# Kernel tuning notes

Hardware: AMD Instinct MI355X
Metric: run time of the kernel (lower is better)

The kernel has to match this reference:

```python
import jax, jax.numpy as jnp
import numpy as np

D = 1024
H = 16
HD = D // H
SCALE = HD ** -0.5


def setup_inputs() -> dict:
    key = jax.random.key(0)
    ks = jax.random.split(key, 5)
    x = jax.random.normal(ks[0], (2, 2048, D), dtype=jnp.float32)
    s = 1.0 / np.sqrt(D)
    W_qkv = jax.random.uniform(ks[1], (D, 3 * D), jnp.float32, -s, s)
    b_qkv = jax.random.uniform(ks[2], (3 * D,), jnp.float32, -s, s)
    W_out = jax.random.uniform(ks[3], (D, D), jnp.float32, -s, s)
    b_out = jax.random.uniform(ks[4], (D,), jnp.float32, -s, s)
    return {"x": x, "W_qkv": W_qkv, "b_qkv": b_qkv, "W_out": W_out, "b_out": b_out}


def reference(x, W_qkv, b_qkv, W_out, b_out):
    B, S, _ = x.shape
    qkv = x @ W_qkv + b_qkv                       # [B,S,3D]
    qkv = qkv.reshape(B, S, 3, H, HD)
    q, k, v = jnp.moveaxis(qkv, 2, 0)             # each [B,S,H,HD]
    # scores: [B,H,S,S]
    scores = jnp.einsum("bshd,bthd->bhst", q, k) * SCALE
    attn = jax.nn.softmax(scores, axis=-1)        # dropout is identity in eval mode
    out = jnp.einsum("bhst,bthd->bshd", attn, v)  # [B,S,H,HD]
    out = out.reshape(B, S, H * HD)
    return out @ W_out + b_out
```

## Files before the change

kernel.cpp:

```cpp
#include <hip/hip_runtime.h>

typedef unsigned short u16;
typedef unsigned int   u32;

using short8 = __attribute__((ext_vector_type(8))) short;
using f32x4  = __attribute__((ext_vector_type(4))) float;

#define QSCALE 0.18033688011112042f

__device__ __forceinline__ u16 f2bf(float f) {
  u32 u = __float_as_uint(f);
  return (u16)((u + 0x8000u) >> 16);
}

__device__ __forceinline__ void gld16(const u16* g, u16* l) {
  __builtin_amdgcn_global_load_lds(
      (const __attribute__((address_space(1))) unsigned int*)g,
      (__attribute__((address_space(3))) unsigned int*)l, 16, 0, 0);
}

__global__ __launch_bounds__(256) void cvt_x(const float* __restrict__ in,
                                             u16* __restrict__ out) {
  int idx = blockIdx.x * 256 + threadIdx.x;
  float4 v = reinterpret_cast<const float4*>(in)[idx];
  ushort4 o;
  o.x = f2bf(v.x); o.y = f2bf(v.y); o.z = f2bf(v.z); o.w = f2bf(v.w);
  reinterpret_cast<ushort4*>(out)[idx] = o;
}

__global__ __launch_bounds__(256) void transpose_w(const float* __restrict__ in,
                                                   u16* __restrict__ out,
                                                   int R, int C) {
  __shared__ u32 s[32][33];
  int c0 = blockIdx.x * 32, r0 = blockIdx.y * 32;
  int j = threadIdx.x & 31, i0 = threadIdx.x >> 5;
#pragma unroll
  for (int p = 0; p < 4; ++p) {
    int i = i0 + p * 8;
    s[i][j] = f2bf(in[(size_t)(r0 + i) * C + c0 + j]);
  }
  __syncthreads();
#pragma unroll
  for (int p = 0; p < 4; ++p) {
    int jj = i0 + p * 8;
    out[(size_t)(c0 + jj) * R + r0 + j] = (u16)s[j][jj];
  }
}

template <int EPI>
__global__ __launch_bounds__(256, 2) void gemm_bt(
    const u16* __restrict__ A, const u16* __restrict__ Bt,
    const float* __restrict__ bias, float* __restrict__ c_out,
    u16* __restrict__ q_out, u16* __restrict__ k_out, u16* __restrict__ vt_out,
    int M, int N, int K) {
  __shared__ __align__(16) u16 As[128 * 32];
  __shared__ __align__(16) u16 Bs[128 * 32];
  const int tid = threadIdx.x;
  const int lane = tid & 63;
  const int wv = tid >> 6;
  const int l16 = lane & 15, quad = lane >> 4;
  const int wm = wv & 1, wn = wv >> 1;
  const int bx = blockIdx.x, by = blockIdx.y;

  const u16* Ab = A + (size_t)by * 128 * K;
  const u16* Bb = Bt + (size_t)bx * 128 * K;

  const f32x4 fzero = {0.0f, 0.0f, 0.0f, 0.0f};
  f32x4 acc[4][4];
#pragma unroll
  for (int i = 0; i < 4; ++i)
#pragma unroll
    for (int j = 0; j < 4; ++j) acc[i][j] = fzero;

  for (int k0 = 0; k0 < K; k0 += 32) {
    __syncthreads();
#pragma unroll
    for (int p = 0; p < 2; ++p) {
      int id = p * 256 + tid;
      int row = id >> 2, blk = id & 3;
      int gc = k0 + ((blk ^ (row & 3)) << 3);
      gld16(Ab + (size_t)row * K + gc, &As[id << 3]);
      gld16(Bb + (size_t)row * K + gc, &Bs[id << 3]);
    }
    __syncthreads();
    short8 af[4], bfr[4];
#pragma unroll
    for (int mi = 0; mi < 4; ++mi) {
      int row = wm * 64 + mi * 16 + l16;
      af[mi] = *reinterpret_cast<const short8*>(&As[row * 32 + ((quad ^ (row & 3)) << 3)]);
    }
#pragma unroll
    for (int ni = 0; ni < 4; ++ni) {
      int row = wn * 64 + ni * 16 + l16;
      bfr[ni] = *reinterpret_cast<const short8*>(&Bs[row * 32 + ((quad ^ (row & 3)) << 3)]);
    }
#pragma unroll
    for (int mi = 0; mi < 4; ++mi)
#pragma unroll
      for (int ni = 0; ni < 4; ++ni)
        acc[mi][ni] = __builtin_amdgcn_mfma_f32_16x16x32_bf16(af[mi], bfr[ni], acc[mi][ni], 0, 0, 0);
  }

#pragma unroll
  for (int mi = 0; mi < 4; ++mi)
#pragma unroll
    for (int ni = 0; ni < 4; ++ni) {
      int col = bx * 128 + wn * 64 + ni * 16 + l16;
      float bv = bias[col];
      int row0 = by * 128 + wm * 64 + mi * 16 + quad * 4;
      if (EPI == 1) {
#pragma unroll
        for (int r = 0; r < 4; ++r)
          c_out[(size_t)(row0 + r) * N + col] = acc[mi][ni][r] + bv;
      } else {
        int which = col >> 10, rem = col & 1023;
        int h = rem >> 6, d = rem & 63;
        int b = row0 >> 11, sq0 = row0 & 2047;
        int bh = (b << 4) + h;
        if (which == 2) {
          ushort4 pk;
          pk.x = f2bf(acc[mi][ni][0] + bv);
          pk.y = f2bf(acc[mi][ni][1] + bv);
          pk.z = f2bf(acc[mi][ni][2] + bv);
          pk.w = f2bf(acc[mi][ni][3] + bv);
          *reinterpret_cast<ushort4*>(&vt_out[(size_t)bh * 131072 + d * 2048 + sq0]) = pk;
        } else {
          size_t base = (size_t)(bh * 2048 + sq0) * 64 + d;
#pragma unroll
          for (int r = 0; r < 4; ++r) {
            float val = acc[mi][ni][r] + bv;
            if (which == 0) q_out[base + r * 64] = f2bf(val * QSCALE);
            else            k_out[base + r * 64] = f2bf(val);
          }
        }
      }
    }
}

__global__ __launch_bounds__(256, 2) void attn(
    const u16* __restrict__ q_buf, const u16* __restrict__ k_buf,
    const u16* __restrict__ vt_buf, u16* __restrict__ o_buf) {
  __shared__ __align__(16) u16 Qs[128 * 64];
  __shared__ __align__(16) u16 Ks[2][64 * 64];
  __shared__ __align__(16) u16 Vts[2][64 * 64];
  __shared__ __align__(16) u16 Pst[4][32 * 72];

  const int tid = threadIdx.x;
  const int lane = tid & 63, w = tid >> 6;
  const int l16 = lane & 15, quad = lane >> 4;
  const int bh = blockIdx.y, q0 = blockIdx.x * 128;

  const u16* qg = q_buf + (size_t)bh * 131072 + q0 * 64;
  const u16* kg = k_buf + (size_t)bh * 131072;
  const u16* vg = vt_buf + (size_t)bh * 131072;

#pragma unroll
  for (int p = 0; p < 4; ++p) {
    int id = p * 256 + tid;
    int row = id >> 3, blk = id & 7;
    gld16(qg + row * 64 + ((blk ^ (row & 7)) << 3), &Qs[id << 3]);
  }
#pragma unroll
  for (int p = 0; p < 2; ++p) {
    int id = p * 256 + tid;
    int row = id >> 3, blk = id & 7;
    gld16(kg + row * 64 + ((blk ^ (row & 7)) << 3), &Ks[0][id << 3]);
    gld16(vg + row * 2048 + ((blk ^ (row & 7)) << 3), &Vts[0][id << 3]);
  }

  const f32x4 fzero = {0.0f, 0.0f, 0.0f, 0.0f};
  f32x4 o_acc[2][4];
  f32x4 o_l[2];
#pragma unroll
  for (int mi = 0; mi < 2; ++mi) {
    o_l[mi] = fzero;
#pragma unroll
    for (int nd = 0; nd < 4; ++nd) o_acc[mi][nd] = fzero;
  }
  short8 ones;
#pragma unroll
  for (int j = 0; j < 8; ++j) ones[j] = (short)0x3F80;

  u16* Pw = Pst[w];
  const int row0 = w * 32 + l16;
  const int row1 = w * 32 + 16 + l16;

  __syncthreads();

  for (int i = 0; i < 32; ++i) {
    const int buf = i & 1;
    if (i + 1 < 32) {
      const int nxt = buf ^ 1;
      const int t1 = (i + 1) * 64;
#pragma unroll
      for (int p = 0; p < 2; ++p) {
        int id = p * 256 + tid;
        int row = id >> 3, blk = id & 7;
        gld16(kg + (t1 + row) * 64 + ((blk ^ (row & 7)) << 3), &Ks[nxt][id << 3]);
        gld16(vg + row * 2048 + t1 + ((blk ^ (row & 7)) << 3), &Vts[nxt][id << 3]);
      }
    }

    f32x4 s_acc[2][4];
#pragma unroll
    for (int mi = 0; mi < 2; ++mi)
#pragma unroll
      for (int ni = 0; ni < 4; ++ni) s_acc[mi][ni] = fzero;
#pragma unroll
    for (int kk = 0; kk < 2; ++kk) {
      short8 a0 = *reinterpret_cast<const short8*>(
          &Qs[row0 * 64 + (((kk * 4 + quad) ^ (row0 & 7)) << 3)]);
      short8 a1 = *reinterpret_cast<const short8*>(
          &Qs[row1 * 64 + (((kk * 4 + quad) ^ (row1 & 7)) << 3)]);
#pragma unroll
      for (int ni = 0; ni < 4; ++ni) {
        int kr = ni * 16 + l16;
        short8 b = *reinterpret_cast<const short8*>(
            &Ks[buf][kr * 64 + (((kk * 4 + quad) ^ (kr & 7)) << 3)]);
        s_acc[0][ni] = __builtin_amdgcn_mfma_f32_16x16x32_bf16(a0, b, s_acc[0][ni], 0, 0, 0);
        s_acc[1][ni] = __builtin_amdgcn_mfma_f32_16x16x32_bf16(a1, b, s_acc[1][ni], 0, 0, 0);
      }
    }

#pragma unroll
    for (int mi = 0; mi < 2; ++mi)
#pragma unroll
      for (int ni = 0; ni < 4; ++ni)
#pragma unroll
        for (int r = 0; r < 4; ++r) {
          float p = __builtin_amdgcn_exp2f(s_acc[mi][ni][r]);
          Pw[(mi * 16 + quad * 4 + r) * 72 + ni * 16 + l16] = f2bf(p);
        }

#pragma unroll
    for (int kk2 = 0; kk2 < 2; ++kk2) {
      short8 pa0 = *reinterpret_cast<const short8*>(&Pw[l16 * 72 + kk2 * 32 + quad * 8]);
      short8 pa1 = *reinterpret_cast<const short8*>(&Pw[(16 + l16) * 72 + kk2 * 32 + quad * 8]);
      o_l[0] = __builtin_amdgcn_mfma_f32_16x16x32_bf16(pa0, ones, o_l[0], 0, 0, 0);
      o_l[1] = __builtin_amdgcn_mfma_f32_16x16x32_bf16(pa1, ones, o_l[1], 0, 0, 0);
#pragma unroll
      for (int nd = 0; nd < 4; ++nd) {
        int d = nd * 16 + l16;
        short8 vb = *reinterpret_cast<const short8*>(
            &Vts[buf][d * 64 + (((kk2 * 4 + quad) ^ (d & 7)) << 3)]);
        o_acc[0][nd] = __builtin_amdgcn_mfma_f32_16x16x32_bf16(pa0, vb, o_acc[0][nd], 0, 0, 0);
        o_acc[1][nd] = __builtin_amdgcn_mfma_f32_16x16x32_bf16(pa1, vb, o_acc[1][nd], 0, 0, 0);
      }
    }

    __syncthreads();
  }

  const int b = bh >> 4, h = bh & 15;
#pragma unroll
  for (int mi = 0; mi < 2; ++mi)
#pragma unroll
    for (int r = 0; r < 4; ++r) {
      int sq = q0 + w * 32 + mi * 16 + quad * 4 + r;
      float inv = 1.0f / o_l[mi][r];
      size_t base = (size_t)(b * 2048 + sq) * 1024 + h * 64;
#pragma unroll
      for (int nd = 0; nd < 4; ++nd)
        o_buf[base + nd * 16 + l16] = f2bf(o_acc[mi][nd][r] * inv);
    }
}

extern "C" void kernel_launch(void* const* d_in, const int* in_sizes, int n_in,
                              void* d_out, int out_size, void* d_ws, size_t ws_size,
                              hipStream_t stream) {
  (void)in_sizes; (void)n_in; (void)out_size; (void)ws_size;
  const float* x     = (const float*)d_in[0];
  const float* W_qkv = (const float*)d_in[1];
  const float* b_qkv = (const float*)d_in[2];
  const float* W_out = (const float*)d_in[3];
  const float* b_out = (const float*)d_in[4];
  float* out = (float*)d_out;

  char* ws = (char*)d_ws;
  u16* x_bf   = (u16*)(ws);
  u16* wqkv_t = (u16*)(ws + 8388608);
  u16* wout_t = (u16*)(ws + 14680064);
  u16* q_buf  = (u16*)(ws + 16777216);
  u16* k_buf  = (u16*)(ws + 25165824);
  u16* vt_buf = (u16*)(ws + 33554432);
  u16* o_bf   = (u16*)(ws + 41943040);

  cvt_x<<<4096, 256, 0, stream>>>(x, x_bf);
  transpose_w<<<dim3(96, 32), 256, 0, stream>>>(W_qkv, wqkv_t, 1024, 3072);
  transpose_w<<<dim3(32, 32), 256, 0, stream>>>(W_out, wout_t, 1024, 1024);
  gemm_bt<0><<<dim3(24, 32), 256, 0, stream>>>(x_bf, wqkv_t, b_qkv, nullptr,
                                               q_buf, k_buf, vt_buf, 4096, 3072, 1024);
  attn<<<dim3(16, 32), 256, 0, stream>>>(q_buf, k_buf, vt_buf, o_bf);
  gemm_bt<1><<<dim3(8, 32), 256, 0, stream>>>(o_bf, wout_t, b_out, out,
                                              nullptr, nullptr, nullptr, 4096, 1024, 1024);
}
```

Measured before the change: 210.6 us.

## Keep attention probabilities in registers via transposed S and fp16 PV MFMA

The attention kernel now computes S transposed (K as the A operand, Q as B), so each lane's exp2 results already sit in the A-operand layout of a 16x16x16 fp16 MFMA. This removes the LDS round-trip for P and the per-wave P staging buffer. V is now stored as fp16 to match. Query tiles shrink to 64 rows with Q fragments held in registers, occupancy is raised to 4 blocks per CU, and the output GEMM uses a 64-row M tile so it launches twice as many blocks. The costs are fp16 range and precision for P and V, and smaller reuse of each K/V tile.

```diff
diff --git a/kernel.cpp b/kernel.cpp
--- a/kernel.cpp
+++ b/kernel.cpp
@@ -5,12 +5,17 @@
 
 using short8 = __attribute__((ext_vector_type(8))) short;
 using f32x4  = __attribute__((ext_vector_type(4))) float;
+using half4  = __attribute__((ext_vector_type(4))) _Float16;
 
 #define QSCALE 0.18033688011112042f
 
 __device__ __forceinline__ u16 f2bf(float f) {
   u32 u = __float_as_uint(f);
   return (u16)((u + 0x8000u) >> 16);
+}
+__device__ __forceinline__ u16 f2h(float f) {
+  _Float16 h = (_Float16)f;
+  return __builtin_bit_cast(u16, h);
 }
 
 __device__ __forceinline__ void gld16(const u16* g, u16* l) {
@@ -47,13 +52,13 @@
   }
 }
 
-template <int EPI>
+template <int EPI, int MT>
 __global__ __launch_bounds__(256, 2) void gemm_bt(
     const u16* __restrict__ A, const u16* __restrict__ Bt,
     const float* __restrict__ bias, float* __restrict__ c_out,
     u16* __restrict__ q_out, u16* __restrict__ k_out, u16* __restrict__ vt_out,
     int M, int N, int K) {
-  __shared__ __align__(16) u16 As[128 * 32];
+  __shared__ __align__(16) u16 As[32 * MT * 32];
   __shared__ __align__(16) u16 Bs[128 * 32];
   const int tid = threadIdx.x;
   const int lane = tid & 63;
@@ -62,31 +67,37 @@
   const int wm = wv & 1, wn = wv >> 1;
   const int bx = blockIdx.x, by = blockIdx.y;
 
-  const u16* Ab = A + (size_t)by * 128 * K;
+  const u16* Ab = A + (size_t)by * (32 * MT) * K;
   const u16* Bb = Bt + (size_t)bx * 128 * K;
 
   const f32x4 fzero = {0.0f, 0.0f, 0.0f, 0.0f};
-  f32x4 acc[4][4];
-#pragma unroll
-  for (int i = 0; i < 4; ++i)
+  f32x4 acc[MT][4];
+#pragma unroll
+  for (int i = 0; i < MT; ++i)
 #pragma unroll
     for (int j = 0; j < 4; ++j) acc[i][j] = fzero;
 
   for (int k0 = 0; k0 < K; k0 += 32) {
     __syncthreads();
+#pragma unroll
+    for (int p = 0; p < MT / 2; ++p) {
+      int id = p * 256 + tid;
+      int row = id >> 2, blk = id & 3;
+      int gc = k0 + ((blk ^ (row & 3)) << 3);
+      gld16(Ab + (size_t)row * K + gc, &As[id << 3]);
+    }
 #pragma unroll
     for (int p = 0; p < 2; ++p) {
       int id = p * 256 + tid;
       int row = id >> 2, blk = id & 3;
       int gc = k0 + ((blk ^ (row & 3)) << 3);
-      gld16(Ab + (size_t)row * K + gc, &As[id << 3]);
       gld16(Bb + (size_t)row * K + gc, &Bs[id << 3]);
     }
     __syncthreads();
-    short8 af[4], bfr[4];
-#pragma unroll
-    for (int mi = 0; mi < 4; ++mi) {
-      int row = wm * 64 + mi * 16 + l16;
+    short8 af[MT], bfr[4];
+#pragma unroll
+    for (int mi = 0; mi < MT; ++mi) {
+      int row = wm * (MT * 16) + mi * 16 + l16;
       af[mi] = *reinterpret_cast<const short8*>(&As[row * 32 + ((quad ^ (row & 3)) << 3)]);
     }
 #pragma unroll
@@ -95,19 +106,19 @@
       bfr[ni] = *reinterpret_cast<const short8*>(&Bs[row * 32 + ((quad ^ (row & 3)) << 3)]);
     }
 #pragma unroll
-    for (int mi = 0; mi < 4; ++mi)
+    for (int mi = 0; mi < MT; ++mi)
 #pragma unroll
       for (int ni = 0; ni < 4; ++ni)
         acc[mi][ni] = __builtin_amdgcn_mfma_f32_16x16x32_bf16(af[mi], bfr[ni], acc[mi][ni], 0, 0, 0);
   }
 
 #pragma unroll
-  for (int mi = 0; mi < 4; ++mi)
+  for (int mi = 0; mi < MT; ++mi)
 #pragma unroll
     for (int ni = 0; ni < 4; ++ni) {
       int col = bx * 128 + wn * 64 + ni * 16 + l16;
       float bv = bias[col];
-      int row0 = by * 128 + wm * 64 + mi * 16 + quad * 4;
+      int row0 = by * (32 * MT) + wm * (MT * 16) + mi * 16 + quad * 4;
       if (EPI == 1) {
 #pragma unroll
         for (int r = 0; r < 4; ++r)
@@ -119,10 +130,10 @@
         int bh = (b << 4) + h;
         if (which == 2) {
           ushort4 pk;
-          pk.x = f2bf(acc[mi][ni][0] + bv);
-          pk.y = f2bf(acc[mi][ni][1] + bv);
-          pk.z = f2bf(acc[mi][ni][2] + bv);
-          pk.w = f2bf(acc[mi][ni][3] + bv);
+          pk.x = f2h(acc[mi][ni][0] + bv);
+          pk.y = f2h(acc[mi][ni][1] + bv);
+          pk.z = f2h(acc[mi][ni][2] + bv);
+          pk.w = f2h(acc[mi][ni][3] + bv);
           *reinterpret_cast<ushort4*>(&vt_out[(size_t)bh * 131072 + d * 2048 + sq0]) = pk;
         } else {
           size_t base = (size_t)(bh * 2048 + sq0) * 64 + d;
@@ -137,55 +148,49 @@
     }
 }
 
-__global__ __launch_bounds__(256, 2) void attn(
+__global__ __launch_bounds__(256, 4) void attn(
     const u16* __restrict__ q_buf, const u16* __restrict__ k_buf,
     const u16* __restrict__ vt_buf, u16* __restrict__ o_buf) {
-  __shared__ __align__(16) u16 Qs[128 * 64];
+  __shared__ __align__(16) u16 Qs[64 * 64];
   __shared__ __align__(16) u16 Ks[2][64 * 64];
   __shared__ __align__(16) u16 Vts[2][64 * 64];
-  __shared__ __align__(16) u16 Pst[4][32 * 72];
 
   const int tid = threadIdx.x;
   const int lane = tid & 63, w = tid >> 6;
   const int l16 = lane & 15, quad = lane >> 4;
-  const int bh = blockIdx.y, q0 = blockIdx.x * 128;
+  const int bh = blockIdx.y, q0 = blockIdx.x * 64;
 
   const u16* qg = q_buf + (size_t)bh * 131072 + q0 * 64;
   const u16* kg = k_buf + (size_t)bh * 131072;
   const u16* vg = vt_buf + (size_t)bh * 131072;
 
 #pragma unroll
-  for (int p = 0; p < 4; ++p) {
-    int id = p * 256 + tid;
-    int row = id >> 3, blk = id & 7;
-    gld16(qg + row * 64 + ((blk ^ (row & 7)) << 3), &Qs[id << 3]);
-  }
-#pragma unroll
   for (int p = 0; p < 2; ++p) {
     int id = p * 256 + tid;
     int row = id >> 3, blk = id & 7;
-    gld16(kg + row * 64 + ((blk ^ (row & 7)) << 3), &Ks[0][id << 3]);
-    gld16(vg + row * 2048 + ((blk ^ (row & 7)) << 3), &Vts[0][id << 3]);
+    int so = (blk ^ (row & 7)) << 3;
+    gld16(qg + row * 64 + so, &Qs[id << 3]);
+    gld16(kg + row * 64 + so, &Ks[0][id << 3]);
+    gld16(vg + row * 2048 + so, &Vts[0][id << 3]);
   }
 
   const f32x4 fzero = {0.0f, 0.0f, 0.0f, 0.0f};
-  f32x4 o_acc[2][4];
-  f32x4 o_l[2];
-#pragma unroll
-  for (int mi = 0; mi < 2; ++mi) {
-    o_l[mi] = fzero;
-#pragma unroll
-    for (int nd = 0; nd < 4; ++nd) o_acc[mi][nd] = fzero;
-  }
-  short8 ones;
-#pragma unroll
-  for (int j = 0; j < 8; ++j) ones[j] = (short)0x3F80;
-
-  u16* Pw = Pst[w];
-  const int row0 = w * 32 + l16;
-  const int row1 = w * 32 + 16 + l16;
+  f32x4 o_acc[4];
+  f32x4 o_l = fzero;
+#pragma unroll
+  for (int nd = 0; nd < 4; ++nd) o_acc[nd] = fzero;
+  half4 ones;
+#pragma unroll
+  for (int j = 0; j < 4; ++j) ones[j] = (_Float16)1.0f;
 
   __syncthreads();
+
+  const int qrow = w * 16 + l16;
+  short8 qb[2];
+#pragma unroll
+  for (int kk = 0; kk < 2; ++kk)
+    qb[kk] = *reinterpret_cast<const short8*>(
+        &Qs[qrow * 64 + (((kk * 4 + quad) ^ (qrow & 7)) << 3)]);
 
   for (int i = 0; i < 32; ++i) {
     const int buf = i & 1;
@@ -196,55 +201,39 @@
       for (int p = 0; p < 2; ++p) {
         int id = p * 256 + tid;
         int row = id >> 3, blk = id & 7;
-        gld16(kg + (t1 + row) * 64 + ((blk ^ (row & 7)) << 3), &Ks[nxt][id << 3]);
-        gld16(vg + row * 2048 + t1 + ((blk ^ (row & 7)) << 3), &Vts[nxt][id << 3]);
-      }
-    }
-
-    f32x4 s_acc[2][4];
-#pragma unroll
-    for (int mi = 0; mi < 2; ++mi)
-#pragma unroll
-      for (int ni = 0; ni < 4; ++ni) s_acc[mi][ni] = fzero;
-#pragma unroll
-    for (int kk = 0; kk < 2; ++kk) {
-      short8 a0 = *reinterpret_cast<const short8*>(
-          &Qs[row0 * 64 + (((kk * 4 + quad) ^ (row0 & 7)) << 3)]);
-      short8 a1 = *reinterpret_cast<const short8*>(
-          &Qs[row1 * 64 + (((kk * 4 + quad) ^ (row1 & 7)) << 3)]);
-#pragma unroll
-      for (int ni = 0; ni < 4; ++ni) {
-        int kr = ni * 16 + l16;
-        short8 b = *reinterpret_cast<const short8*>(
+        int so = (blk ^ (row & 7)) << 3;
+        gld16(kg + (t1 + row) * 64 + so, &Ks[nxt][id << 3]);
+        gld16(vg + row * 2048 + t1 + so, &Vts[nxt][id << 3]);
+      }
+    }
+
+    f32x4 s[4];
+#pragma unroll
+    for (int ti = 0; ti < 4; ++ti) s[ti] = fzero;
+#pragma unroll
+    for (int kk = 0; kk < 2; ++kk)
+#pragma unroll
+      for (int ti = 0; ti < 4; ++ti) {
+        int kr = ti * 16 + l16;
+        short8 ka = *reinterpret_cast<const short8*>(
             &Ks[buf][kr * 64 + (((kk * 4 + quad) ^ (kr & 7)) << 3)]);
-        s_acc[0][ni] = __builtin_amdgcn_mfma_f32_16x16x32_bf16(a0, b, s_acc[0][ni], 0, 0, 0);
-        s_acc[1][ni] = __builtin_amdgcn_mfma_f32_16x16x32_bf16(a1, b, s_acc[1][ni], 0, 0, 0);
-      }
-    }
-
-#pragma unroll
-    for (int mi = 0; mi < 2; ++mi)
-#pragma unroll
-      for (int ni = 0; ni < 4; ++ni)
-#pragma unroll
-        for (int r = 0; r < 4; ++r) {
-          float p = __builtin_amdgcn_exp2f(s_acc[mi][ni][r]);
-          Pw[(mi * 16 + quad * 4 + r) * 72 + ni * 16 + l16] = f2bf(p);
-        }
-
-#pragma unroll
-    for (int kk2 = 0; kk2 < 2; ++kk2) {
-      short8 pa0 = *reinterpret_cast<const short8*>(&Pw[l16 * 72 + kk2 * 32 + quad * 8]);
-      short8 pa1 = *reinterpret_cast<const short8*>(&Pw[(16 + l16) * 72 + kk2 * 32 + quad * 8]);
-      o_l[0] = __builtin_amdgcn_mfma_f32_16x16x32_bf16(pa0, ones, o_l[0], 0, 0, 0);
-      o_l[1] = __builtin_amdgcn_mfma_f32_16x16x32_bf16(pa1, ones, o_l[1], 0, 0, 0);
+        s[ti] = __builtin_amdgcn_mfma_f32_16x16x32_bf16(ka, qb[kk], s[ti], 0, 0, 0);
+      }
+
+#pragma unroll
+    for (int ti = 0; ti < 4; ++ti) {
+      half4 pa;
+#pragma unroll
+      for (int j = 0; j < 4; ++j)
+        pa[j] = (_Float16)__builtin_amdgcn_exp2f(s[ti][j]);
+      o_l = __builtin_amdgcn_mfma_f32_16x16x16f16(pa, ones, o_l, 0, 0, 0);
 #pragma unroll
       for (int nd = 0; nd < 4; ++nd) {
         int d = nd * 16 + l16;
-        short8 vb = *reinterpret_cast<const short8*>(
-            &Vts[buf][d * 64 + (((kk2 * 4 + quad) ^ (d & 7)) << 3)]);
-        o_acc[0][nd] = __builtin_amdgcn_mfma_f32_16x16x32_bf16(pa0, vb, o_acc[0][nd], 0, 0, 0);
-        o_acc[1][nd] = __builtin_amdgcn_mfma_f32_16x16x32_bf16(pa1, vb, o_acc[1][nd], 0, 0, 0);
+        int tloc = ti * 16 + quad * 4;
+        const half4 vb = *reinterpret_cast<const half4*>(
+            &Vts[buf][d * 64 + ((((tloc >> 3) ^ (d & 7)) << 3) | (tloc & 7))]);
+        o_acc[nd] = __builtin_amdgcn_mfma_f32_16x16x16f16(pa, vb, o_acc[nd], 0, 0, 0);
       }
     }
 
@@ -253,16 +242,14 @@
 
   const int b = bh >> 4, h = bh & 15;
 #pragma unroll
-  for (int mi = 0; mi < 2; ++mi)
-#pragma unroll
-    for (int r = 0; r < 4; ++r) {
-      int sq = q0 + w * 32 + mi * 16 + quad * 4 + r;
-      float inv = 1.0f / o_l[mi][r];
-      size_t base = (size_t)(b * 2048 + sq) * 1024 + h * 64;
-#pragma unroll
-      for (int nd = 0; nd < 4; ++nd)
-        o_buf[base + nd * 16 + l16] = f2bf(o_acc[mi][nd][r] * inv);
-    }
+  for (int r = 0; r < 4; ++r) {
+    int sq = q0 + w * 16 + quad * 4 + r;
+    float inv = 1.0f / o_l[r];
+    size_t base = (size_t)(b * 2048 + sq) * 1024 + h * 64;
+#pragma unroll
+    for (int nd = 0; nd < 4; ++nd)
+      o_buf[base + nd * 16 + l16] = f2bf(o_acc[nd][r] * inv);
+  }
 }
 
 extern "C" void kernel_launch(void* const* d_in, const int* in_sizes, int n_in,
@@ -288,9 +275,9 @@
   cvt_x<<<4096, 256, 0, stream>>>(x, x_bf);
   transpose_w<<<dim3(96, 32), 256, 0, stream>>>(W_qkv, wqkv_t, 1024, 3072);
   transpose_w<<<dim3(32, 32), 256, 0, stream>>>(W_out, wout_t, 1024, 1024);
-  gemm_bt<0><<<dim3(24, 32), 256, 0, stream>>>(x_bf, wqkv_t, b_qkv, nullptr,
-                                               q_buf, k_buf, vt_buf, 4096, 3072, 1024);
-  attn<<<dim3(16, 32), 256, 0, stream>>>(q_buf, k_buf, vt_buf, o_bf);
-  gemm_bt<1><<<dim3(8, 32), 256, 0, stream>>>(o_bf, wout_t, b_out, out,
-                                              nullptr, nullptr, nullptr, 4096, 1024, 1024);
-}
+  gemm_bt<0, 4><<<dim3(24, 32), 256, 0, stream>>>(x_bf, wqkv_t, b_qkv, nullptr,
+                                                  q_buf, k_buf, vt_buf, 4096, 3072, 1024);
+  attn<<<dim3(32, 32), 256, 0, stream>>>(q_buf, k_buf, vt_buf, o_bf);
+  gemm_bt<1, 2><<<dim3(8, 64), 256, 0, stream>>>(o_bf, wout_t, b_out, out,
+                                                 nullptr, nullptr, nullptr, 4096, 1024, 1024);
+}
```

After: 194.0 us. 7.9% less time.
